# Performance work log

Measured on AMD Instinct MI355X. Metric: run time of the kernel, lower is better.

The kernel has to match this reference:

```python
import jax, jax.numpy as jnp
import numpy as np

V, E, H, L, T_MAX = 50257, 384, 6, 6, 256
HS = E // H  # 64
LN_EPS = 1e-5


def _ln(x, g, b):
    mu = jnp.mean(x, axis=-1, keepdims=True)
    var = jnp.mean(jnp.square(x - mu), axis=-1, keepdims=True)
    return (x - mu) * jax.lax.rsqrt(var + LN_EPS) * g + b


def setup_inputs() -> dict:
    key = jax.random.key(0)
    ks = jax.random.split(key, 24)
    B, T = 16, 256
    s_emb = 1.0 / np.sqrt(E)
    inp = {
        'idx': jax.random.randint(ks[0], (B, T), 0, V),
        'targets': jax.random.randint(ks[1], (B, T), 0, V),
        'tok_emb': jax.random.normal(ks[2], (V, E), jnp.float32) * 0.02,
        'pos_emb': jax.random.normal(ks[3], (V, E), jnp.float32) * 0.02,
        'Wq': jax.random.normal(ks[4], (L, E, E), jnp.float32) * s_emb,
        'Wk': jax.random.normal(ks[5], (L, E, E), jnp.float32) * s_emb,
        'Wv': jax.random.normal(ks[6], (L, E, E), jnp.float32) * s_emb,
        'Wproj': jax.random.normal(ks[7], (L, E, E), jnp.float32) * s_emb,
        'bproj': jnp.zeros((L, E), jnp.float32),
        'W1': jax.random.normal(ks[8], (L, E, 4 * E), jnp.float32) * s_emb,
        'b1': jnp.zeros((L, 4 * E), jnp.float32),
        'W2': jax.random.normal(ks[9], (L, 4 * E, E), jnp.float32) * (0.5 * s_emb),
        'b2': jnp.zeros((L, E), jnp.float32),
        'ln1_g': jnp.ones((L, E), jnp.float32), 'ln1_b': jnp.zeros((L, E), jnp.float32),
        'ln2_g': jnp.ones((L, E), jnp.float32), 'ln2_b': jnp.zeros((L, E), jnp.float32),
        'lnf_g': jnp.ones((E,), jnp.float32), 'lnf_b': jnp.zeros((E,), jnp.float32),
        'Whead': jax.random.normal(ks[10], (E, V), jnp.float32) * s_emb,
        'bhead': jnp.zeros((V,), jnp.float32),
    }
    return inp


def _forward(idx, targets, tok_emb, pos_emb, Wq, Wk, Wv, Wproj, bproj,
             W1, b1, W2, b2, ln1_g, ln1_b, ln2_g, ln2_b, lnf_g, lnf_b, Whead, bhead):
    B, T = idx.shape
    x = tok_emb[idx] + pos_emb[:T]                      # [B,T,E]
    causal = jnp.tril(jnp.ones((T, T), bool))           # tril mask
    scale = E ** (-0.5)                                 # NOTE: scaled by n_embd, as in source
    for l in range(L):
        h = _ln(x, ln1_g[l], ln1_b[l])
        q = (h @ Wq[l]).reshape(B, T, H, HS)
        k = (h @ Wk[l]).reshape(B, T, H, HS)
        v = (h @ Wv[l]).reshape(B, T, H, HS)
        wei = jnp.einsum('bqhd,bkhd->bhqk', q, k) * scale
        wei = jnp.where(causal, wei, -jnp.inf)
        wei = jax.nn.softmax(wei, axis=-1)              # dropout: eval mode (identity)
        att = jnp.einsum('bhqk,bkhd->bqhd', wei, v).reshape(B, T, E)
        x = x + att @ Wproj[l] + bproj[l]
        h2 = _ln(x, ln2_g[l], ln2_b[l])
        x = x + jax.nn.relu(h2 @ W1[l] + b1[l]) @ W2[l] + b2[l]
    x = _ln(x, lnf_g, lnf_b)
    logits = x @ Whead + bhead                          # [B,T,V]
    logp = jax.nn.log_softmax(logits, axis=-1)
    loss = -jnp.mean(jnp.take_along_axis(logp, targets[..., None], axis=-1))
    return logits, loss


def reference(idx, targets, tok_emb, pos_emb, Wq, Wk, Wv, Wproj, bproj,
              W1, b1, W2, b2, ln1_g, ln1_b, ln2_g, ln2_b, lnf_g, lnf_b, Whead, bhead):
    return _forward(idx, targets, tok_emb, pos_emb, Wq, Wk, Wv, Wproj, bproj,
                    W1, b1, W2, b2, ln1_g, ln1_b, ln2_g, ln2_b, lnf_g, lnf_b, Whead, bhead)
```

## Files before the change

kernel.cpp:

```cpp
#include <hip/hip_runtime.h>

#define NL 6
#define EMB 384
#define NH 6
#define HSZ 64
#define TT 256
#define NTOK 4096
#define VOC 50257
#define VOCP 50304
#define FF 1536
#define QKVW 1152
#define NCH 393

typedef __attribute__((ext_vector_type(8))) short bf16x8;
typedef __attribute__((ext_vector_type(4))) float f32x4;

__device__ __forceinline__ short f2bf(float f) {
  unsigned u = __float_as_uint(f);
  u = (u + 0x7fffu + ((u >> 16) & 1u)) >> 16;
  return (short)u;
}

__device__ __forceinline__ int swz16(int b) {
  return b ^ (((((b >> 6) ^ (b >> 8)) & 1) << 4) | (((b >> 7) & 1) << 5));
}

__device__ __forceinline__ void gl16(const void* g, void* l) {
  __builtin_amdgcn_global_load_lds(
      (const __attribute__((address_space(1))) unsigned*)g,
      (__attribute__((address_space(3))) unsigned*)l, 16, 0, 0);
}

__global__ void embed_k(const int* __restrict__ idx, const float* __restrict__ tok,
                        const float* __restrict__ pos, float* __restrict__ x) {
  int row = blockIdx.x, col = threadIdx.x;
  int t = idx[row];
  x[(size_t)row * EMB + col] = tok[(size_t)t * EMB + col] + pos[(size_t)(row & 255) * EMB + col];
}

__global__ __launch_bounds__(256) void tcast_k(const float* __restrict__ src, short* __restrict__ dst,
                                               int K, int N, long sstr, long dstr) {
  src += (size_t)blockIdx.z * sstr;
  dst += (size_t)blockIdx.z * dstr;
  __shared__ float tile[32][33];
  int lx = threadIdx.x & 31, ly = threadIdx.x >> 5;
  int k0 = blockIdx.y << 5, n0 = blockIdx.x << 5;
#pragma unroll
  for (int j = 0; j < 4; ++j) {
    int k = k0 + ly + (j << 3), n = n0 + lx;
    tile[ly + (j << 3)][lx] = (n < N) ? src[(size_t)k * N + n] : 0.f;
  }
  __syncthreads();
#pragma unroll
  for (int j = 0; j < 4; ++j) {
    int n = n0 + ly + (j << 3), k = k0 + lx;
    dst[(size_t)n * K + k] = f2bf(tile[lx][ly + (j << 3)]);
  }
}

__global__ __launch_bounds__(256) void ln_k(const float* __restrict__ x, const float* __restrict__ g,
                                            const float* __restrict__ b, short* __restrict__ out) {
  int wave = threadIdx.x >> 6, lane = threadIdx.x & 63;
  int row = (blockIdx.x << 2) + wave;
  const float* p = x + (size_t)row * EMB;
  float v[6]; float s = 0.f;
#pragma unroll
  for (int j = 0; j < 6; ++j) { v[j] = p[lane + (j << 6)]; s += v[j]; }
#pragma unroll
  for (int o = 32; o; o >>= 1) s += __shfl_xor(s, o, 64);
  float mu = s * (1.f / EMB);
  float q = 0.f;
#pragma unroll
  for (int j = 0; j < 6; ++j) { float d = v[j] - mu; q += d * d; }
#pragma unroll
  for (int o = 32; o; o >>= 1) q += __shfl_xor(q, o, 64);
  float rstd = rsqrtf(q * (1.f / EMB) + 1e-5f);
  short* op = out + (size_t)row * EMB;
#pragma unroll
  for (int j = 0; j < 6; ++j) {
    int c = lane + (j << 6);
    op[c] = f2bf((v[j] - mu) * rstd * g[c] + b[c]);
  }
}

__global__ __launch_bounds__(256) void vtrans_k(const short* __restrict__ qkv, short* __restrict__ vt) {
  int bh = blockIdx.y; int b = bh / NH, h = bh % NH;
  int t0 = blockIdx.x << 6;
  __shared__ short tile[64][72];
  int tid = threadIdx.x;
#pragma unroll
  for (int pass = 0; pass < 2; ++pass) {
    int tl = pass * 32 + (tid >> 3);
    int d0 = (tid & 7) << 3;
    uint4 v = *(const uint4*)&qkv[((size_t)(b * TT + t0 + tl)) * QKVW + 2 * EMB + h * HSZ + d0];
    *(uint4*)&tile[tl][d0] = v;
  }
  __syncthreads();
  int d = tid >> 2, tc = (tid & 3) << 4;
  short* dst = &vt[((size_t)bh * 64 + d) * TT + t0 + tc];
#pragma unroll
  for (int j = 0; j < 16; ++j) dst[j] = tile[tc + j][d];
}

template <int KFB>
__device__ __forceinline__ void attn_body(const short* __restrict__ qkv,
                                          const short* __restrict__ vt,
                                          short* __restrict__ att,
                                          short (*P)[260], int qt, int bh, int tid) {
  const float SCALE = 0.051031036307982884f;
  int b = bh / NH, h = bh % NH;
  int w = tid >> 6, lane = tid & 63;
  int lr = lane & 15, g = lane >> 4;
  int qbase = qt * 64 + w * 16;

  const short* qrow = qkv + (size_t)(b * TT + qbase + lr) * QKVW + h * HSZ;
  bf16x8 qa0 = *(const bf16x8*)(qrow + g * 8);
  bf16x8 qa1 = *(const bf16x8*)(qrow + 32 + g * 8);

  f32x4 zero = {0.f, 0.f, 0.f, 0.f};
  f32x4 s[KFB];
#pragma unroll
  for (int kf = 0; kf < KFB; ++kf) s[kf] = zero;
#pragma unroll
  for (int kf = 0; kf < KFB; ++kf) {
    const short* krow = qkv + (size_t)(b * TT + kf * 16 + lr) * QKVW + EMB + h * HSZ;
    bf16x8 kb0 = *(const bf16x8*)(krow + g * 8);
    bf16x8 kb1 = *(const bf16x8*)(krow + 32 + g * 8);
    s[kf] = __builtin_amdgcn_mfma_f32_16x16x32_bf16(qa0, kb0, s[kf], 0, 0, 0);
    s[kf] = __builtin_amdgcn_mfma_f32_16x16x32_bf16(qa1, kb1, s[kf], 0, 0, 0);
  }

#pragma unroll
  for (int i = 0; i < 4; ++i) {
    int qg = qbase + g * 4 + i;
    float m = -1e30f;
#pragma unroll
    for (int kf = 0; kf < KFB; ++kf) {
      float v = s[kf][i] * SCALE;
      if (kf * 16 + lr > qg) v = -1e30f;
      s[kf][i] = v;
      m = fmaxf(m, v);
    }
#pragma unroll
    for (int o = 8; o; o >>= 1) m = fmaxf(m, __shfl_xor(m, o, 64));
    float sum = 0.f;
#pragma unroll
    for (int kf = 0; kf < KFB; ++kf) {
      float e = __expf(s[kf][i] - m);
      s[kf][i] = e;
      sum += e;
    }
#pragma unroll
    for (int o = 8; o; o >>= 1) sum += __shfl_xor(sum, o, 64);
    float inv = 1.f / sum;
#pragma unroll
    for (int kf = 0; kf < KFB; ++kf)
      P[w * 16 + g * 4 + i][kf * 16 + lr] = f2bf(s[kf][i] * inv);
  }

  f32x4 o4[4];
#pragma unroll
  for (int nf = 0; nf < 4; ++nf) o4[nf] = zero;
  const short* vbase = vt + (size_t)bh * 64 * TT;
#pragma unroll
  for (int ks = 0; ks < KFB / 2; ++ks) {
    bf16x8 pa = *(const bf16x8*)&P[w * 16 + lr][ks * 32 + g * 8];
#pragma unroll
    for (int nf = 0; nf < 4; ++nf) {
      bf16x8 vb = *(const bf16x8*)(vbase + (size_t)(nf * 16 + lr) * TT + ks * 32 + g * 8);
      o4[nf] = __builtin_amdgcn_mfma_f32_16x16x32_bf16(pa, vb, o4[nf], 0, 0, 0);
    }
  }
#pragma unroll
  for (int nf = 0; nf < 4; ++nf)
#pragma unroll
    for (int i = 0; i < 4; ++i)
      att[(size_t)(b * TT + qbase + g * 4 + i) * EMB + h * HSZ + nf * 16 + lr] = f2bf(o4[nf][i]);
}

__global__ __launch_bounds__(256) void attn_k(const short* __restrict__ qkv,
                                              const short* __restrict__ vt,
                                              short* __restrict__ att) {
  __shared__ short P[64][260];
  int qt = blockIdx.x, bh = blockIdx.y, tid = threadIdx.x;
  if (qt == 0)      attn_body<4>(qkv, vt, att, P, 0, bh, tid);
  else if (qt == 1) attn_body<8>(qkv, vt, att, P, 1, bh, tid);
  else if (qt == 2) attn_body<12>(qkv, vt, att, P, 2, bh, tid);
  else              attn_body<16>(qkv, vt, att, P, 3, bh, tid);
}

#define GM_QKV 0
#define GM_FC1 4
#define GM_HEAD 5

template <int MODE>
__global__ __launch_bounds__(256) void gemm_k(
    const short* __restrict__ Ag, const short* __restrict__ Btg, void* Cg,
    const float* __restrict__ bias, const float* resid,
    int K, int lda, int ldb, int ldc, float scale,
    float* __restrict__ pm, float* __restrict__ ps) {
  __shared__ alignas(1024) char smem[2 * 2 * 128 * 32 * 2];
  short* sA = (short*)smem;
  short* sB = (short*)(smem + 16384);
  int tid = threadIdx.x;
  int bm = blockIdx.x, bn = blockIdx.y;
  int wave = tid >> 6, lane = tid & 63;
  int wm = wave >> 1, wn = wave & 1;
  int lr = lane & 15, kq = lane >> 4;
  size_t lda2 = (size_t)lda * 2, ldb2 = (size_t)ldb * 2;

  int p = wave * 1024 + lane * 16;
  int q = swz16(p);
  int srow = q >> 6, scb = q & 63;
  const char* gA = (const char*)Ag + (size_t)(bm * 128 + srow) * lda2 + scb;
  const char* gB = (const char*)Btg + (size_t)(bn * 128 + srow) * ldb2 + scb;
  char* lA0 = (char*)sA + wave * 1024; char* lA1 = lA0 + 4096;
  char* lB0 = (char*)sB + wave * 1024; char* lB1 = lB0 + 4096;

  const char* apf[4]; const char* bpf[4];
#pragma unroll
  for (int f = 0; f < 4; ++f) {
    int La = (wm * 64 + f * 16 + lr) * 64 + kq * 16;
    apf[f] = (const char*)sA + swz16(La);
    int Lb = (wn * 64 + f * 16 + lr) * 64 + kq * 16;
    bpf[f] = (const char*)sB + swz16(Lb);
  }

  f32x4 zero = {0.f, 0.f, 0.f, 0.f};
  f32x4 acc[4][4];
#pragma unroll
  for (int i = 0; i < 4; ++i)
#pragma unroll
    for (int j = 0; j < 4; ++j) acc[i][j] = zero;

  gl16(gA, lA0); gl16(gA + 64 * lda2, lA1);
  gl16(gB, lB0); gl16(gB + 64 * ldb2, lB1);
  __syncthreads();

  int nt = K >> 5;
  for (int t = 0; t < nt; ++t) {
    int cur = (t & 1) << 13, nxt = (~t & 1) << 13;
    if (t + 1 < nt) {
      const char* ga2 = gA + (size_t)(t + 1) * 64;
      const char* gb2 = gB + (size_t)(t + 1) * 64;
      gl16(ga2, lA0 + nxt); gl16(ga2 + 64 * lda2, lA1 + nxt);
      gl16(gb2, lB0 + nxt); gl16(gb2 + 64 * ldb2, lB1 + nxt);
    }
    bf16x8 af[4], bfr[4];
#pragma unroll
    for (int f = 0; f < 4; ++f) {
      af[f] = *(const bf16x8*)(apf[f] + cur);
      bfr[f] = *(const bf16x8*)(bpf[f] + cur);
    }
#pragma unroll
    for (int i = 0; i < 4; ++i)
#pragma unroll
      for (int j = 0; j < 4; ++j)
        acc[i][j] = __builtin_amdgcn_mfma_f32_16x16x32_bf16(af[i], bfr[j], acc[i][j], 0, 0, 0);
    __syncthreads();
  }

  int row0 = bm * 128 + wm * 64 + (kq << 2);
  int col0 = bn * 128 + wn * 64 + lr;

  if constexpr (MODE == GM_QKV) {
    short* C = (short*)Cg;
#pragma unroll
    for (int fm = 0; fm < 4; ++fm)
#pragma unroll
      for (int fn = 0; fn < 4; ++fn) {
        int c = col0 + fn * 16;
#pragma unroll
        for (int i = 0; i < 4; ++i)
          C[(size_t)(row0 + fm * 16 + i) * ldc + c] = f2bf(acc[fm][fn][i]);
      }
  } else if constexpr (MODE == GM_FC1) {
    short* C = (short*)Cg;
#pragma unroll
    for (int fm = 0; fm < 4; ++fm)
#pragma unroll
      for (int fn = 0; fn < 4; ++fn) {
        int c = col0 + fn * 16;
        float bv = bias[c];
#pragma unroll
        for (int i = 0; i < 4; ++i)
          C[(size_t)(row0 + fm * 16 + i) * ldc + c] = f2bf(fmaxf(acc[fm][fn][i] + bv, 0.f));
      }
  } else if constexpr (MODE == GM_HEAD) {
    __shared__ float redm[2][2][64];
    __shared__ float reds[2][2][64];
    float* C = (float*)Cg;
    bool okv[4]; float bv[4];
#pragma unroll
    for (int fn = 0; fn < 4; ++fn) {
      int c = col0 + fn * 16;
      okv[fn] = c < VOC;
      bv[fn] = okv[fn] ? bias[c] : 0.f;
    }
#pragma unroll
    for (int fm = 0; fm < 4; ++fm)
#pragma unroll
      for (int fn = 0; fn < 4; ++fn)
#pragma unroll
        for (int i = 0; i < 4; ++i) acc[fm][fn][i] += bv[fn];
#pragma unroll
    for (int fm = 0; fm < 4; ++fm)
#pragma unroll
      for (int i = 0; i < 4; ++i) {
        float v0 = okv[0] ? acc[fm][0][i] : -1e30f;
        float v1 = okv[1] ? acc[fm][1][i] : -1e30f;
        float v2 = okv[2] ? acc[fm][2][i] : -1e30f;
        float v3 = okv[3] ? acc[fm][3][i] : -1e30f;
        float mx = fmaxf(fmaxf(v0, v1), fmaxf(v2, v3));
#pragma unroll
        for (int o = 8; o; o >>= 1) mx = fmaxf(mx, __shfl_xor(mx, o, 64));
        float sm = __expf(v0 - mx) + __expf(v1 - mx) + __expf(v2 - mx) + __expf(v3 - mx);
#pragma unroll
        for (int o = 8; o; o >>= 1) sm += __shfl_xor(sm, o, 64);
        if (lr == 0) {
          int rl = fm * 16 + (kq << 2) + i;
          redm[wm][wn][rl] = mx; reds[wm][wn][rl] = sm;
        }
      }
    __syncthreads();
    if (tid < 128) {
      int wmm = tid >> 6, rl = tid & 63;
      float m0 = redm[wmm][0][rl], m1 = redm[wmm][1][rl];
      float s0 = reds[wmm][0][rl], s1 = reds[wmm][1][rl];
      float M = fmaxf(m0, m1);
      float S = s0 * __expf(m0 - M) + s1 * __expf(m1 - M);
      int r = bm * 128 + wmm * 64 + rl;
      pm[(size_t)r * NCH + bn] = M;
      ps[(size_t)r * NCH + bn] = S;
    }
    float (*cst)[132] = reinterpret_cast<float(*)[132]>(smem);
    int colbase = bn * 128;
#pragma unroll
    for (int c = 0; c < 4; ++c) {
      __syncthreads();
      if (wm == (c >> 1)) {
        int fmb = (c & 1) * 2;
#pragma unroll
        for (int f2 = 0; f2 < 2; ++f2)
#pragma unroll
          for (int fn = 0; fn < 4; ++fn)
#pragma unroll
            for (int i = 0; i < 4; ++i)
              cst[f2 * 16 + kq * 4 + i][wn * 64 + fn * 16 + lr] = acc[fmb + f2][fn][i];
      }
      __syncthreads();
      int rowg = bm * 128 + c * 32;
#pragma unroll
      for (int pp = 0; pp < 16; ++pp) {
        int idx = pp * 256 + tid;
        int rw = idx >> 7, cc = idx & 127;
        int gc = colbase + cc;
        if (gc < VOC)
          __builtin_nontemporal_store(cst[rw][cc], &C[(size_t)(rowg + rw) * VOC + gc]);
      }
    }
  }
}

__global__ __launch_bounds__(256) void gemm64_k(
    const short* __restrict__ Ag, const short* __restrict__ Btg, float* __restrict__ C,
    const float* __restrict__ bias, const float* __restrict__ resid,
    int K, int lda, int ldb, int ldc) {
  __shared__ alignas(1024) short sA[2 * 64 * 32];
  __shared__ alignas(1024) short sB[2 * 64 * 32];
  int tid = threadIdx.x;
  int bm = blockIdx.x, bn = blockIdx.y;
  int wave = tid >> 6, lane = tid & 63;
  int wm = wave >> 1, wn = wave & 1;
  int lr = lane & 15, kq = lane >> 4;
  size_t lda2 = (size_t)lda * 2, ldb2 = (size_t)ldb * 2;

  int p = wave * 1024 + lane * 16;
  int q = swz16(p);
  int srow = q >> 6, scb = q & 63;
  const char* gA = (const char*)Ag + (size_t)(bm * 64 + srow) * lda2 + scb;
  const char* gB = (const char*)Btg + (size_t)(bn * 64 + srow) * ldb2 + scb;
  char* lA0 = (char*)sA + wave * 1024;
  char* lB0 = (char*)sB + wave * 1024;

  const char* apf[2]; const char* bpf[2];
#pragma unroll
  for (int f = 0; f < 2; ++f) {
    apf[f] = (const char*)sA + swz16((wm * 32 + f * 16 + lr) * 64 + kq * 16);
    bpf[f] = (const char*)sB + swz16((wn * 32 + f * 16 + lr) * 64 + kq * 16);
  }

  f32x4 zero = {0.f, 0.f, 0.f, 0.f};
  f32x4 acc[2][2];
#pragma unroll
  for (int i = 0; i < 2; ++i)
#pragma unroll
    for (int j = 0; j < 2; ++j) acc[i][j] = zero;

  gl16(gA, lA0);
  gl16(gB, lB0);
  __syncthreads();

  int nt = K >> 5;
  for (int t = 0; t < nt; ++t) {
    int cur = (t & 1) << 12, nxt = (~t & 1) << 12;
    if (t + 1 < nt) {
      gl16(gA + (size_t)(t + 1) * 64, lA0 + nxt);
      gl16(gB + (size_t)(t + 1) * 64, lB0 + nxt);
    }
    bf16x8 af[2], bfr[2];
#pragma unroll
    for (int f = 0; f < 2; ++f) {
      af[f] = *(const bf16x8*)(apf[f] + cur);
      bfr[f] = *(const bf16x8*)(bpf[f] + cur);
    }
#pragma unroll
    for (int i = 0; i < 2; ++i)
#pragma unroll
      for (int j = 0; j < 2; ++j)
        acc[i][j] = __builtin_amdgcn_mfma_f32_16x16x32_bf16(af[i], bfr[j], acc[i][j], 0, 0, 0);
    __syncthreads();
  }

  int row0 = bm * 64 + wm * 32 + (kq << 2);
  int col0 = bn * 64 + wn * 32 + lr;
#pragma unroll
  for (int fm = 0; fm < 2; ++fm)
#pragma unroll
    for (int fn = 0; fn < 2; ++fn) {
      int c = col0 + fn * 16;
      float bv = bias[c];
#pragma unroll
      for (int i = 0; i < 4; ++i) {
        size_t o = (size_t)(row0 + fm * 16 + i) * ldc + c;
        C[o] = resid[o] + acc[fm][fn][i] + bv;
      }
    }
}

__global__ __launch_bounds__(256) void lsecomb_k(const float* __restrict__ pm, const float* __restrict__ ps,
                                                 const float* __restrict__ logits, const int* __restrict__ tgt,
                                                 float* __restrict__ rowloss) {
  int wave = threadIdx.x >> 6, lane = threadIdx.x & 63;
  int r = (blockIdx.x << 2) + wave;
  float m = -1e30f, s = 0.f;
  for (int i = lane; i < NCH; i += 64) {
    float bm = pm[(size_t)r * NCH + i], bs = ps[(size_t)r * NCH + i];
    float M = fmaxf(m, bm);
    s = s * __expf(m - M) + bs * __expf(bm - M);
    m = M;
  }
#pragma unroll
  for (int o = 32; o; o >>= 1) {
    float mo = __shfl_xor(m, o, 64), so = __shfl_xor(s, o, 64);
    float M = fmaxf(m, mo);
    s = s * __expf(m - M) + so * __expf(mo - M);
    m = M;
  }
  if (lane == 0) rowloss[r] = m + __logf(s) - logits[(size_t)r * VOC + tgt[r]];
}

__global__ __launch_bounds__(256) void loss_final_k(const float* __restrict__ rowloss,
                                                    float* __restrict__ out) {
  __shared__ float sb[256];
  int tid = threadIdx.x;
  float s = 0.f;
  for (int i = tid; i < NTOK; i += 256) s += rowloss[i];
  sb[tid] = s;
  __syncthreads();
  for (int o = 128; o; o >>= 1) {
    if (tid < o) sb[tid] += sb[tid + o];
    __syncthreads();
  }
  if (tid == 0) out[0] = sb[0] * (1.f / NTOK);
}

extern "C" void kernel_launch(void* const* d_in, const int* in_sizes, int n_in,
                              void* d_out, int out_size, void* d_ws, size_t ws_size,
                              hipStream_t stream) {
  const int* idx = (const int*)d_in[0];
  const int* tgt = (const int*)d_in[1];
  const float* tok = (const float*)d_in[2];
  const float* pos = (const float*)d_in[3];
  const float* Wq = (const float*)d_in[4];
  const float* Wk = (const float*)d_in[5];
  const float* Wv = (const float*)d_in[6];
  const float* Wp = (const float*)d_in[7];
  const float* bp = (const float*)d_in[8];
  const float* W1 = (const float*)d_in[9];
  const float* b1 = (const float*)d_in[10];
  const float* W2 = (const float*)d_in[11];
  const float* b2 = (const float*)d_in[12];
  const float* ln1g = (const float*)d_in[13];
  const float* ln1b = (const float*)d_in[14];
  const float* ln2g = (const float*)d_in[15];
  const float* ln2b = (const float*)d_in[16];
  const float* lnfg = (const float*)d_in[17];
  const float* lnfb = (const float*)d_in[18];
  const float* Wh = (const float*)d_in[19];
  const float* bh = (const float*)d_in[20];

  char* wp = (char*)d_ws;
  auto take = [&](size_t elems, size_t esz) {
    void* r = (void*)wp;
    wp += (elems * esz + 255) & ~(size_t)255;
    return r;
  };
  short* wqkv_t = (short*)take((size_t)NL * QKVW * EMB, 2);
  short* wproj_t = (short*)take((size_t)NL * EMB * EMB, 2);
  short* w1_t = (short*)take((size_t)NL * FF * EMB, 2);
  short* w2_t = (short*)take((size_t)NL * EMB * FF, 2);
  short* whead_t = (short*)take((size_t)VOCP * EMB, 2);
  float* x = (float*)take((size_t)NTOK * EMB, 4);
  short* hb = (short*)take((size_t)NTOK * EMB, 2);
  short* qkv = (short*)take((size_t)NTOK * QKVW, 2);
  float* sc = (float*)take((size_t)96 * TT * TT, 4);
  short* vt = (short*)take((size_t)96 * 64 * TT, 2);
  short* att = (short*)take((size_t)NTOK * EMB, 2);
  short* f1 = (short*)take((size_t)NTOK * FF, 2);
  float* rl = (float*)take((size_t)NTOK, 4);

  float* pm = sc;
  float* ps = sc + (size_t)NTOK * NCH;

  tcast_k<<<dim3(12, 12, NL), 256, 0, stream>>>(Wq, wqkv_t, EMB, EMB, (long)EMB * EMB, (long)QKVW * EMB);
  tcast_k<<<dim3(12, 12, NL), 256, 0, stream>>>(Wk, wqkv_t + EMB * EMB, EMB, EMB, (long)EMB * EMB, (long)QKVW * EMB);
  tcast_k<<<dim3(12, 12, NL), 256, 0, stream>>>(Wv, wqkv_t + 2 * EMB * EMB, EMB, EMB, (long)EMB * EMB, (long)QKVW * EMB);
  tcast_k<<<dim3(12, 12, NL), 256, 0, stream>>>(Wp, wproj_t, EMB, EMB, (long)EMB * EMB, (long)EMB * EMB);
  tcast_k<<<dim3(48, 12, NL), 256, 0, stream>>>(W1, w1_t, EMB, FF, (long)EMB * FF, (long)FF * EMB);
  tcast_k<<<dim3(12, 48, NL), 256, 0, stream>>>(W2, w2_t, FF, EMB, (long)FF * EMB, (long)EMB * FF);
  tcast_k<<<dim3(VOCP / 32, 12, 1), 256, 0, stream>>>(Wh, whead_t, EMB, VOC, 0, 0);

  embed_k<<<NTOK, EMB, 0, stream>>>(idx, tok, pos, x);

  for (int l = 0; l < NL; ++l) {
    ln_k<<<NTOK / 4, 256, 0, stream>>>(x, ln1g + l * EMB, ln1b + l * EMB, hb);
    gemm_k<GM_QKV><<<dim3(32, 9), 256, 0, stream>>>(hb, wqkv_t + (size_t)l * QKVW * EMB, qkv,
        nullptr, nullptr, EMB, EMB, EMB, QKVW, 0.f, nullptr, nullptr);
    vtrans_k<<<dim3(4, 96), 256, 0, stream>>>(qkv, vt);
    attn_k<<<dim3(4, 96), 256, 0, stream>>>(qkv, vt, att);
    gemm64_k<<<dim3(64, 6), 256, 0, stream>>>(att, wproj_t + (size_t)l * EMB * EMB, x,
        bp + l * EMB, x, EMB, EMB, EMB, EMB);
    ln_k<<<NTOK / 4, 256, 0, stream>>>(x, ln2g + l * EMB, ln2b + l * EMB, hb);
    gemm_k<GM_FC1><<<dim3(32, 12), 256, 0, stream>>>(hb, w1_t + (size_t)l * FF * EMB, f1,
        b1 + l * FF, nullptr, EMB, EMB, EMB, FF, 0.f, nullptr, nullptr);
    gemm64_k<<<dim3(64, 6), 256, 0, stream>>>(f1, w2_t + (size_t)l * EMB * FF, x,
        b2 + l * EMB, x, FF, FF, FF, EMB);
  }

  ln_k<<<NTOK / 4, 256, 0, stream>>>(x, lnfg, lnfb, hb);
  gemm_k<GM_HEAD><<<dim3(32, NCH), 256, 0, stream>>>(hb, whead_t, (float*)d_out,
      bh, nullptr, EMB, EMB, EMB, VOC, 0.f, pm, ps);
  lsecomb_k<<<NTOK / 4, 256, 0, stream>>>(pm, ps, (const float*)d_out, tgt, rl);
  loss_final_k<<<1, 256, 0, stream>>>(rl, (float*)d_out + (size_t)NTOK * VOC);
}
```

Before: 970.8 us.

## Fuse V transpose into QKV GEMM epilogue and deepen head GEMM prefetch

```diff
diff --git a/kernel.cpp b/kernel.cpp
--- a/kernel.cpp
+++ b/kernel.cpp
@@ -83,25 +83,6 @@
   }
 }
 
-__global__ __launch_bounds__(256) void vtrans_k(const short* __restrict__ qkv, short* __restrict__ vt) {
-  int bh = blockIdx.y; int b = bh / NH, h = bh % NH;
-  int t0 = blockIdx.x << 6;
-  __shared__ short tile[64][72];
-  int tid = threadIdx.x;
-#pragma unroll
-  for (int pass = 0; pass < 2; ++pass) {
-    int tl = pass * 32 + (tid >> 3);
-    int d0 = (tid & 7) << 3;
-    uint4 v = *(const uint4*)&qkv[((size_t)(b * TT + t0 + tl)) * QKVW + 2 * EMB + h * HSZ + d0];
-    *(uint4*)&tile[tl][d0] = v;
-  }
-  __syncthreads();
-  int d = tid >> 2, tc = (tid & 3) << 4;
-  short* dst = &vt[((size_t)bh * 64 + d) * TT + t0 + tc];
-#pragma unroll
-  for (int j = 0; j < 16; ++j) dst[j] = tile[tc + j][d];
-}
-
 template <int KFB>
 __device__ __forceinline__ void attn_body(const short* __restrict__ qkv,
                                           const short* __restrict__ vt,
@@ -198,7 +179,7 @@
     const short* __restrict__ Ag, const short* __restrict__ Btg, void* Cg,
     const float* __restrict__ bias, const float* resid,
     int K, int lda, int ldb, int ldc, float scale,
-    float* __restrict__ pm, float* __restrict__ ps) {
+    float* __restrict__ pm, float* __restrict__ ps, short* __restrict__ vtp) {
   __shared__ alignas(1024) char smem[2 * 2 * 128 * 32 * 2];
   short* sA = (short*)smem;
   short* sB = (short*)(smem + 16384);
@@ -233,31 +214,54 @@
 #pragma unroll
     for (int j = 0; j < 4; ++j) acc[i][j] = zero;
 
-  gl16(gA, lA0); gl16(gA + 64 * lda2, lA1);
-  gl16(gB, lB0); gl16(gB + 64 * ldb2, lB1);
-  __syncthreads();
+  auto STAGE = [&](int t, int bufoff) {
+    const char* ga2 = gA + (size_t)t * 64;
+    const char* gb2 = gB + (size_t)t * 64;
+    gl16(ga2, lA0 + bufoff); gl16(ga2 + 64 * lda2, lA1 + bufoff);
+    gl16(gb2, lB0 + bufoff); gl16(gb2 + 64 * ldb2, lB1 + bufoff);
+  };
 
   int nt = K >> 5;
-  for (int t = 0; t < nt; ++t) {
-    int cur = (t & 1) << 13, nxt = (~t & 1) << 13;
-    if (t + 1 < nt) {
-      const char* ga2 = gA + (size_t)(t + 1) * 64;
-      const char* gb2 = gB + (size_t)(t + 1) * 64;
-      gl16(ga2, lA0 + nxt); gl16(ga2 + 64 * lda2, lA1 + nxt);
-      gl16(gb2, lB0 + nxt); gl16(gb2 + 64 * ldb2, lB1 + nxt);
-    }
-    bf16x8 af[4], bfr[4];
-#pragma unroll
-    for (int f = 0; f < 4; ++f) {
-      af[f] = *(const bf16x8*)(apf[f] + cur);
-      bfr[f] = *(const bf16x8*)(bpf[f] + cur);
-    }
-#pragma unroll
-    for (int i = 0; i < 4; ++i)
-#pragma unroll
-      for (int j = 0; j < 4; ++j)
-        acc[i][j] = __builtin_amdgcn_mfma_f32_16x16x32_bf16(af[i], bfr[j], acc[i][j], 0, 0, 0);
+  if constexpr (MODE == GM_HEAD) {
+    STAGE(0, 0);
+    STAGE(1, 8192);
+    for (int t = 0; t < nt; ++t) {
+      int cur = (t & 1) << 13;
+      if (t + 1 < nt) { asm volatile("s_waitcnt vmcnt(4)\ns_barrier" ::: "memory"); }
+      else            { asm volatile("s_waitcnt vmcnt(0)\ns_barrier" ::: "memory"); }
+      bf16x8 af[4], bfr[4];
+#pragma unroll
+      for (int f = 0; f < 4; ++f) {
+        af[f] = *(const bf16x8*)(apf[f] + cur);
+        bfr[f] = *(const bf16x8*)(bpf[f] + cur);
+      }
+#pragma unroll
+      for (int i = 0; i < 4; ++i)
+#pragma unroll
+        for (int j = 0; j < 4; ++j)
+          acc[i][j] = __builtin_amdgcn_mfma_f32_16x16x32_bf16(af[i], bfr[j], acc[i][j], 0, 0, 0);
+      asm volatile("s_waitcnt lgkmcnt(0)\ns_barrier" ::: "memory");
+      if (t + 2 < nt) STAGE(t + 2, cur);
+    }
+  } else {
+    STAGE(0, 0);
     __syncthreads();
+    for (int t = 0; t < nt; ++t) {
+      int cur = (t & 1) << 13, nxt = (~t & 1) << 13;
+      if (t + 1 < nt) STAGE(t + 1, nxt);
+      bf16x8 af[4], bfr[4];
+#pragma unroll
+      for (int f = 0; f < 4; ++f) {
+        af[f] = *(const bf16x8*)(apf[f] + cur);
+        bfr[f] = *(const bf16x8*)(bpf[f] + cur);
+      }
+#pragma unroll
+      for (int i = 0; i < 4; ++i)
+#pragma unroll
+        for (int j = 0; j < 4; ++j)
+          acc[i][j] = __builtin_amdgcn_mfma_f32_16x16x32_bf16(af[i], bfr[j], acc[i][j], 0, 0, 0);
+      __syncthreads();
+    }
   }
 
   int row0 = bm * 128 + wm * 64 + (kq << 2);
@@ -271,8 +275,17 @@
       for (int fn = 0; fn < 4; ++fn) {
         int c = col0 + fn * 16;
 #pragma unroll
-        for (int i = 0; i < 4; ++i)
-          C[(size_t)(row0 + fm * 16 + i) * ldc + c] = f2bf(acc[fm][fn][i]);
+        for (int i = 0; i < 4; ++i) {
+          int r = row0 + fm * 16 + i;
+          short val = f2bf(acc[fm][fn][i]);
+          C[(size_t)r * ldc + c] = val;
+          if (c >= 2 * EMB) {
+            int dg = c - 2 * EMB;
+            int h = dg >> 6, d = dg & 63;
+            int b = r >> 8, tt = r & 255;
+            vtp[(((size_t)(b * NH + h) * 64 + d) << 8) + tt] = val;
+          }
+        }
       }
   } else if constexpr (MODE == GM_FC1) {
     short* C = (short*)Cg;
@@ -536,21 +549,20 @@
   for (int l = 0; l < NL; ++l) {
     ln_k<<<NTOK / 4, 256, 0, stream>>>(x, ln1g + l * EMB, ln1b + l * EMB, hb);
     gemm_k<GM_QKV><<<dim3(32, 9), 256, 0, stream>>>(hb, wqkv_t + (size_t)l * QKVW * EMB, qkv,
-        nullptr, nullptr, EMB, EMB, EMB, QKVW, 0.f, nullptr, nullptr);
-    vtrans_k<<<dim3(4, 96), 256, 0, stream>>>(qkv, vt);
+        nullptr, nullptr, EMB, EMB, EMB, QKVW, 0.f, nullptr, nullptr, vt);
     attn_k<<<dim3(4, 96), 256, 0, stream>>>(qkv, vt, att);
     gemm64_k<<<dim3(64, 6), 256, 0, stream>>>(att, wproj_t + (size_t)l * EMB * EMB, x,
         bp + l * EMB, x, EMB, EMB, EMB, EMB);
     ln_k<<<NTOK / 4, 256, 0, stream>>>(x, ln2g + l * EMB, ln2b + l * EMB, hb);
     gemm_k<GM_FC1><<<dim3(32, 12), 256, 0, stream>>>(hb, w1_t + (size_t)l * FF * EMB, f1,
-        b1 + l * FF, nullptr, EMB, EMB, EMB, FF, 0.f, nullptr, nullptr);
+        b1 + l * FF, nullptr, EMB, EMB, EMB, FF, 0.f, nullptr, nullptr, nullptr);
     gemm64_k<<<dim3(64, 6), 256, 0, stream>>>(f1, w2_t + (size_t)l * EMB * FF, x,
         b2 + l * EMB, x, FF, FF, FF, EMB);
   }
 
   ln_k<<<NTOK / 4, 256, 0, stream>>>(x, lnfg, lnfb, hb);
   gemm_k<GM_HEAD><<<dim3(32, NCH), 256, 0, stream>>>(hb, whead_t, (float*)d_out,
-      bh, nullptr, EMB, EMB, EMB, VOC, 0.f, pm, ps);
+      bh, nullptr, EMB, EMB, EMB, VOC, 0.f, pm, ps, nullptr);
   lsecomb_k<<<NTOK / 4, 256, 0, stream>>>(pm, ps, (const float*)d_out, tgt, rl);
   loss_final_k<<<1, 256, 0, stream>>>(rl, (float*)d_out + (size_t)NTOK * VOC);
 }
```

After: 1.007 ms. +3.8%, slower.
